# Performance work log

Measured on AMD Instinct MI355X. Metric: run time of the kernel, lower is better.

## Reference

```python
import jax, jax.numpy as jnp
import numpy as np
import math

N_HEADS = 16
DIM = 1024
D_HEAD = DIM // N_HEADS
BS, QLEN = 2, 2048


def setup_inputs() -> dict:
    key = jax.random.key(0)
    ks = jax.random.split(key, 10)
    s = 0.02
    return {
        "input": jax.random.normal(ks[0], (BS, QLEN, DIM), dtype=jnp.float32),
        "mask": jnp.ones((BS, QLEN), dtype=jnp.int32),
        "q_w": jax.random.normal(ks[1], (DIM, DIM), dtype=jnp.float32) * s,
        "q_b": jax.random.normal(ks[2], (DIM,), dtype=jnp.float32) * s,
        "k_w": jax.random.normal(ks[3], (DIM, DIM), dtype=jnp.float32) * s,
        "k_b": jax.random.normal(ks[4], (DIM,), dtype=jnp.float32) * s,
        "v_w": jax.random.normal(ks[5], (DIM, DIM), dtype=jnp.float32) * s,
        "v_b": jax.random.normal(ks[6], (DIM,), dtype=jnp.float32) * s,
        "o_w": jax.random.normal(ks[7], (DIM, DIM), dtype=jnp.float32) * s,
        "o_b": jax.random.normal(ks[8], (DIM,), dtype=jnp.float32) * s,
    }


def _shape(x, bs):
    # (bs, len, dim) -> (bs, heads, len, d_head)
    return x.reshape(bs, -1, N_HEADS, D_HEAD).transpose(0, 2, 1, 3)


def reference(input, mask, q_w, q_b, k_w, k_b, v_w, v_b, o_w, o_b):
    bs, qlen, dim = input.shape
    # projections (torch Linear: x @ W^T + b)
    q = _shape(input @ q_w.T + q_b, bs)
    k = _shape(input @ k_w.T + k_b, bs)
    v = _shape(input @ v_w.T + v_b, bs)
    q = q / math.sqrt(D_HEAD)
    # scores: (bs, heads, qlen, klen)
    scores = jnp.einsum("bhqd,bhkd->bhqk", q, k)
    pad = (mask == 0)[:, None, None, :]  # (bs,1,1,klen)
    scores = jnp.where(pad, -jnp.inf, scores)
    weights = jax.nn.softmax(scores.astype(jnp.float32), axis=-1).astype(scores.dtype)
    # dropout p=0.0 (eval) -> identity
    context = jnp.einsum("bhqk,bhkd->bhqd", weights, v)
    context = context.transpose(0, 2, 1, 3).reshape(bs, qlen, dim)
    return context @ o_w.T + o_b
```

## Files before the change

kernel.cpp:

```cpp
#include <hip/hip_runtime.h>


#define BS    2
#define QLEN  2048
#define DIM   1024
#define NH    16
#define DH    64
#define MTOK  (BS * QLEN)

#define QSCALE 0.18033688011112042f

typedef __attribute__((ext_vector_type(8))) short short8;
typedef __attribute__((ext_vector_type(4))) float float4_t;
typedef __attribute__((ext_vector_type(4))) int   int4_t;

__device__ __forceinline__ ushort f2bf(float f) {
    unsigned u = __float_as_uint(f);
    return (ushort)((u + 0x7fffu + ((u >> 16) & 1u)) >> 16);
}
__device__ __forceinline__ short8 pack8(float4 a0, float4 a1) {
    short8 r;
    r[0] = (short)f2bf(a0.x); r[1] = (short)f2bf(a0.y);
    r[2] = (short)f2bf(a0.z); r[3] = (short)f2bf(a0.w);
    r[4] = (short)f2bf(a1.x); r[5] = (short)f2bf(a1.y);
    r[6] = (short)f2bf(a1.z); r[7] = (short)f2bf(a1.w);
    return r;
}

__device__ __forceinline__ void glds16(const void* g, void* l) {
    __builtin_amdgcn_global_load_lds(
        (const __attribute__((address_space(1))) unsigned int*)g,
        (__attribute__((address_space(3))) unsigned int*)l, 16, 0, 0);
}

#define QBAR() do { asm volatile("" ::: "memory");                            \
                    __builtin_amdgcn_s_barrier();                             \
                    asm volatile("" ::: "memory"); } while (0)

__global__ __launch_bounds__(256) void conv_all(
    const float* __restrict__ x,  const float* __restrict__ qw,
    const float* __restrict__ kw, const float* __restrict__ vw,
    const float* __restrict__ ow,
    ushort* __restrict__ Xbf, ushort* __restrict__ Wbf)
{
    const int blk = blockIdx.x;
    const float* s; ushort* d; size_t base;
    if (blk < 4096)      { s = x;  d = Xbf;             base = (size_t)blk * 1024; }
    else if (blk < 5120) { s = qw; d = Wbf;             base = (size_t)(blk - 4096) * 1024; }
    else if (blk < 6144) { s = kw; d = Wbf + 1048576;   base = (size_t)(blk - 5120) * 1024; }
    else if (blk < 7168) { s = vw; d = Wbf + 2097152;   base = (size_t)(blk - 6144) * 1024; }
    else                 { s = ow; d = Wbf + 3145728;   base = (size_t)(blk - 7168) * 1024; }
    const size_t i = base + threadIdx.x * 4;
    float4 v = *(const float4*)(s + i);
    ushort4 o;
    o.x = f2bf(v.x); o.y = f2bf(v.y); o.z = f2bf(v.z); o.w = f2bf(v.w);
    *(ushort4*)(d + i) = o;
}

__global__ __launch_bounds__(256) void transpose_v(
    const ushort* __restrict__ Vrow, ushort* __restrict__ Vt)
{
    __shared__ ushort T[64][72];
    const int tid  = threadIdx.x;
    const int tile = blockIdx.x;
    const int bh   = blockIdx.y;
    const int b = bh >> 4, h = bh & 15;

    #pragma unroll
    for (int rep = 0; rep < 2; ++rep) {
        int ch = tid + rep * 256;
        int tok = ch >> 3, seg = ch & 7;
        uint4 v = *(const uint4*)(Vrow + (size_t)(b * QLEN + tile * 64 + tok) * DIM
                                        + h * DH + seg * 8);
        *(uint4*)&T[tok][seg * 8] = v;
    }
    __syncthreads();
    #pragma unroll
    for (int rep = 0; rep < 2; ++rep) {
        int ch = tid + rep * 256;
        int dim = ch >> 3, tseg = ch & 7;
        ushort t0 = T[tseg * 8 + 0][dim], t1 = T[tseg * 8 + 1][dim];
        ushort t2 = T[tseg * 8 + 2][dim], t3 = T[tseg * 8 + 3][dim];
        ushort t4 = T[tseg * 8 + 4][dim], t5 = T[tseg * 8 + 5][dim];
        ushort t6 = T[tseg * 8 + 6][dim], t7 = T[tseg * 8 + 7][dim];
        uint4 o;
        o.x = (unsigned)t0 | ((unsigned)t1 << 16);
        o.y = (unsigned)t2 | ((unsigned)t3 << 16);
        o.z = (unsigned)t4 | ((unsigned)t5 << 16);
        o.w = (unsigned)t6 | ((unsigned)t7 << 16);
        *(uint4*)(Vt + (size_t)bh * DH * QLEN + (size_t)dim * QLEN
                      + tile * 64 + tseg * 8) = o;
    }
}

__global__ __launch_bounds__(256) void gemm_qkv(
    const ushort* __restrict__ A, const ushort* __restrict__ Bw,
    const float* __restrict__ bias0, const float* __restrict__ bias1,
    const float* __restrict__ bias2,
    ushort* __restrict__ outQ, ushort* __restrict__ outK, ushort* __restrict__ outVt)
{
    __shared__ ushort As[3][128 * 32];
    __shared__ ushort Bs[3][128 * 32];
    const int tid  = threadIdx.x;
    const int w    = tid >> 6;
    const int lane = tid & 63;
    const int r15  = lane & 15;
    const int quad = lane >> 4;
    const int xcd = blockIdx.x & 7;
    const int lid = blockIdx.x >> 3;
    const int brow = (xcd & 3) * 8  + (lid & 7);
    const int bcol = (xcd >> 2) * 12 + (lid >> 3);
    const int wrow = (w >> 1) * 64;
    const int wcol = (w & 1) * 64;
    const int K = DIM;

    float4_t acc[4][4];
    #pragma unroll
    for (int i = 0; i < 4; ++i)
        #pragma unroll
        for (int j = 0; j < 4; ++j)
            acc[i][j] = (float4_t){0.f, 0.f, 0.f, 0.f};

    int chS[2];
    const ushort* gaS[2];
    const ushort* gbS[2];
    #pragma unroll
    for (int rep = 0; rep < 2; ++rep) {
        const int ch  = w * 128 + rep * 64 + lane;
        const int row = ch >> 2;
        const int g   = (ch & 3) ^ ((row >> 1) & 3);
        chS[rep] = ch;
        gaS[rep] = A  + (size_t)(brow * 128 + row) * K + g * 8;
        gbS[rep] = Bw + (size_t)(bcol * 128 + row) * K + g * 8;
    }
    const int ph = (quad ^ ((r15 >> 1) & 3)) * 8;

#define QKV_STAGE(PS, KOFF) do {                                              \
    _Pragma("unroll")                                                         \
    for (int rep = 0; rep < 2; ++rep) {                                       \
        glds16(gaS[rep] + (KOFF), &As[PS][chS[rep] * 8]);                     \
        glds16(gbS[rep] + (KOFF), &Bs[PS][chS[rep] * 8]);                     \
    }                                                                         \
} while (0)

#define QKV_COMP(PC) do {                                                     \
    short8 af[4], bf[4];                                                      \
    _Pragma("unroll")                                                         \
    for (int ms = 0; ms < 4; ++ms)                                            \
        af[ms] = *(const short8*)&As[PC][(wrow + ms * 16 + r15) * 32 + ph];   \
    _Pragma("unroll")                                                         \
    for (int ns = 0; ns < 4; ++ns)                                            \
        bf[ns] = *(const short8*)&Bs[PC][(wcol + ns * 16 + r15) * 32 + ph];   \
    _Pragma("unroll")                                                         \
    for (int ms = 0; ms < 4; ++ms)                                            \
        _Pragma("unroll")                                                     \
        for (int ns = 0; ns < 4; ++ns)                                        \
            acc[ms][ns] = __builtin_amdgcn_mfma_f32_16x16x32_bf16(            \
                af[ms], bf[ns], acc[ms][ns], 0, 0, 0);                        \
} while (0)

#define QKV_STEP(PC, PS, KOFF2) do {                                          \
    QKV_STAGE(PS, KOFF2);                                                     \
    asm volatile("s_waitcnt vmcnt(8)" ::: "memory");                          \
    __builtin_amdgcn_s_barrier();                                             \
    asm volatile("" ::: "memory");                                            \
    QKV_COMP(PC);                                                             \
    QBAR();                                                                   \
} while (0)

    QKV_STAGE(0, 0);
    QKV_STAGE(1, 32);

    for (int t0 = 0; t0 < 30; t0 += 3) {
        const int kb = t0 * 32;
        QKV_STEP(0, 2, kb + 64);
        QKV_STEP(1, 0, kb + 96);
        QKV_STEP(2, 1, kb + 128);
    }
    asm volatile("s_waitcnt vmcnt(4)" ::: "memory");
    __builtin_amdgcn_s_barrier();
    asm volatile("" ::: "memory");
    QKV_COMP(0);
    QBAR();
    asm volatile("s_waitcnt vmcnt(0)" ::: "memory");
    __builtin_amdgcn_s_barrier();
    asm volatile("" ::: "memory");
    QKV_COMP(1);

#undef QKV_STEP
#undef QKV_COMP
#undef QKV_STAGE

    #pragma unroll
    for (int ms = 0; ms < 4; ++ms) {
        const int rowg = brow * 128 + wrow + ms * 16 + quad * 4;
        #pragma unroll
        for (int ns = 0; ns < 4; ++ns) {
            const int colg = bcol * 128 + wcol + ns * 16 + r15;
            if (colg < 1024) {
                const float bb = bias0[colg];
                #pragma unroll
                for (int r = 0; r < 4; ++r)
                    outQ[(size_t)(rowg + r) * 1024 + colg] =
                        f2bf((acc[ms][ns][r] + bb) * QSCALE);
            } else if (colg < 2048) {
                const float bb = bias1[colg - 1024];
                #pragma unroll
                for (int r = 0; r < 4; ++r)
                    outK[(size_t)(rowg + r) * 1024 + (colg - 1024)] =
                        f2bf(acc[ms][ns][r] + bb);
            } else {
                const int vcol = colg - 2048;
                const int hh = vcol >> 6, dd = vcol & 63;
                const float bb = bias2[vcol];
                const int bidx = rowg >> 11;
                const int tloc = rowg & 2047;
                ushort4 o4;
                o4.x = f2bf(acc[ms][ns][0] + bb);
                o4.y = f2bf(acc[ms][ns][1] + bb);
                o4.z = f2bf(acc[ms][ns][2] + bb);
                o4.w = f2bf(acc[ms][ns][3] + bb);
                *(ushort4*)&outVt[((size_t)(bidx * 16 + hh) * 64 + dd) * QLEN + tloc] = o4;
            }
        }
    }
}

__global__ __launch_bounds__(256) void gemm_o(
    const ushort* __restrict__ A, const ushort* __restrict__ Bw,
    const float* __restrict__ bias, float* __restrict__ Out)
{
    __shared__ ushort As[2][128 * 64];
    __shared__ ushort Bs[2][64 * 64];
    const int tid  = threadIdx.x;
    const int w    = tid >> 6;
    const int lane = tid & 63;
    const int r15  = lane & 15;
    const int quad = lane >> 4;
    const int xcd = blockIdx.x & 7;
    const int lid = blockIdx.x >> 3;
    const int brow = (xcd & 3) * 8 + (lid & 7);
    const int bcol = (xcd >> 2) * 8 + (lid >> 3);
    const int wrow = w * 32;
    const int K = DIM;

    float4_t acc[2][4];
    #pragma unroll
    for (int i = 0; i < 2; ++i)
        #pragma unroll
        for (int j = 0; j < 4; ++j)
            acc[i][j] = (float4_t){0.f, 0.f, 0.f, 0.f};

    int chA[4];  const ushort* gaS[4];
    #pragma unroll
    for (int rep = 0; rep < 4; ++rep) {
        const int ch  = w * 256 + rep * 64 + lane;
        const int row = ch >> 3;
        const int g   = (ch & 7) ^ (row & 7);
        chA[rep] = ch;
        gaS[rep] = A + (size_t)(brow * 128 + row) * K + g * 8;
    }
    int chB[2];  const ushort* gbS[2];
    #pragma unroll
    for (int rep = 0; rep < 2; ++rep) {
        const int ch  = w * 128 + rep * 64 + lane;
        const int row = ch >> 3;
        const int g   = (ch & 7) ^ (row & 7);
        chB[rep] = ch;
        gbS[rep] = Bw + (size_t)(bcol * 64 + row) * K + g * 8;
    }
    const int xg = r15 & 7;

    #pragma unroll
    for (int rep = 0; rep < 4; ++rep)
        glds16(gaS[rep], &As[0][chA[rep] * 8]);
    #pragma unroll
    for (int rep = 0; rep < 2; ++rep)
        glds16(gbS[rep], &Bs[0][chB[rep] * 8]);
    __syncthreads();

    int p = 0;
    for (int k0 = 0; k0 < K; k0 += 64) {
        if (k0 + 64 < K) {
            #pragma unroll
            for (int rep = 0; rep < 4; ++rep)
                glds16(gaS[rep] + k0 + 64, &As[p ^ 1][chA[rep] * 8]);
            #pragma unroll
            for (int rep = 0; rep < 2; ++rep)
                glds16(gbS[rep] + k0 + 64, &Bs[p ^ 1][chB[rep] * 8]);
        }
        #pragma unroll
        for (int hh = 0; hh < 2; ++hh) {
            const int ph = ((hh * 4 + quad) ^ xg) * 8;
            short8 af[2], bf[4];
            #pragma unroll
            for (int ms = 0; ms < 2; ++ms)
                af[ms] = *(const short8*)&As[p][(wrow + ms * 16 + r15) * 64 + ph];
            #pragma unroll
            for (int ns = 0; ns < 4; ++ns)
                bf[ns] = *(const short8*)&Bs[p][(ns * 16 + r15) * 64 + ph];
            #pragma unroll
            for (int ms = 0; ms < 2; ++ms)
                #pragma unroll
                for (int ns = 0; ns < 4; ++ns)
                    acc[ms][ns] = __builtin_amdgcn_mfma_f32_16x16x32_bf16(
                        af[ms], bf[ns], acc[ms][ns], 0, 0, 0);
        }
        __syncthreads();
        p ^= 1;
    }

    #pragma unroll
    for (int ms = 0; ms < 2; ++ms) {
        const int rowg = brow * 128 + wrow + ms * 16 + quad * 4;
        #pragma unroll
        for (int ns = 0; ns < 4; ++ns) {
            const int colg = bcol * 64 + ns * 16 + r15;
            const float bb = bias[colg];
            #pragma unroll
            for (int r = 0; r < 4; ++r)
                Out[(size_t)(rowg + r) * 1024 + colg] = acc[ms][ns][r] + bb;
        }
    }
}

__global__ __launch_bounds__(256) void gemm_f32in_bf16out(
    const float* __restrict__ X, const float* __restrict__ W,
    const float* __restrict__ B, ushort* __restrict__ Out,
    int M, int N, int K, float scale)
{
    const int lane = threadIdx.x & 63;
    const int wid  = (blockIdx.x * blockDim.x + threadIdx.x) >> 6;
    const int tilesN = N >> 4;
    const int tm = wid / tilesN;
    const int tn = wid - tm * tilesN;
    const int r15  = lane & 15;
    const int quad = lane >> 4;

    const float* xp = X + (size_t)(tm * 16 + r15) * K + quad * 8;
    const float* wp = W + (size_t)(tn * 16 + r15) * K + quad * 8;

    float4_t acc = {0.f, 0.f, 0.f, 0.f};
    for (int k0 = 0; k0 < K; k0 += 32) {
        float4 a0 = *(const float4*)(xp + k0);
        float4 a1 = *(const float4*)(xp + k0 + 4);
        float4 b0 = *(const float4*)(wp + k0);
        float4 b1 = *(const float4*)(wp + k0 + 4);
        acc = __builtin_amdgcn_mfma_f32_16x16x32_bf16(pack8(a0, a1), pack8(b0, b1), acc, 0, 0, 0);
    }
    const int col  = tn * 16 + r15;
    const float bias = B[col];
    const int row0 = tm * 16 + quad * 4;
    #pragma unroll
    for (int r = 0; r < 4; ++r)
        Out[(size_t)(row0 + r) * N + col] = f2bf((acc[r] + bias) * scale);
}

__global__ __launch_bounds__(256) void gemm_bf16in_f32out(
    const ushort* __restrict__ X, const float* __restrict__ W,
    const float* __restrict__ B, float* __restrict__ Out,
    int M, int N, int K)
{
    const int lane = threadIdx.x & 63;
    const int wid  = (blockIdx.x * blockDim.x + threadIdx.x) >> 6;
    const int tilesN = N >> 4;
    const int tm = wid / tilesN;
    const int tn = wid - tm * tilesN;
    const int r15  = lane & 15;
    const int quad = lane >> 4;

    const ushort* xp = X + (size_t)(tm * 16 + r15) * K + quad * 8;
    const float*  wp = W + (size_t)(tn * 16 + r15) * K + quad * 8;

    float4_t acc = {0.f, 0.f, 0.f, 0.f};
    for (int k0 = 0; k0 < K; k0 += 32) {
        short8 a = *(const short8*)(xp + k0);
        float4 b0 = *(const float4*)(wp + k0);
        float4 b1 = *(const float4*)(wp + k0 + 4);
        acc = __builtin_amdgcn_mfma_f32_16x16x32_bf16(a, pack8(b0, b1), acc, 0, 0, 0);
    }
    const int col  = tn * 16 + r15;
    const float bias = B[col];
    const int row0 = tm * 16 + quad * 4;
    #pragma unroll
    for (int r = 0; r < 4; ++r)
        Out[(size_t)(row0 + r) * N + col] = acc[r] + bias;
}

__global__ __launch_bounds__(256, 2) void flash_attn(
    const ushort* __restrict__ Qb, const ushort* __restrict__ Kb,
    const ushort* __restrict__ Vt, const int* __restrict__ mask,
    ushort* __restrict__ Cb)
{
    __shared__ __align__(16) ushort Ks[2][64][64];
    __shared__ __align__(16) ushort Vs[4][64][64];
    __shared__ __align__(16) float  Mb[QLEN];

    const int tid  = threadIdx.x;
    const int w    = tid >> 6;
    const int lane = tid & 63;
    const int r15  = lane & 15;
    const int quad = lane >> 4;
    const int flat = blockIdx.x;
    const int xcd  = flat & 7;
    const int j    = flat >> 3;
    const int bh   = xcd + 8 * (j >> 4);
    const int qt   = j & 15;
    const int b = bh >> 4, h = bh & 15;

    {
        const int4* m4 = (const int4*)(mask + b * QLEN);
        #pragma unroll
        for (int rep = 0; rep < 2; ++rep) {
            const int idx = tid + rep * 256;
            int4 mv = m4[idx];
            float4 o;
            o.x = mv.x ? 0.f : -INFINITY;
            o.y = mv.y ? 0.f : -INFINITY;
            o.z = mv.z ? 0.f : -INFINITY;
            o.w = mv.w ? 0.f : -INFINITY;
            *(float4*)&Mb[idx * 4] = o;
        }
    }

    const int qbase = qt * 128 + w * 32;
    const ushort* qp = Qb + (size_t)(b * QLEN + qbase + r15) * DIM + h * DH + quad * 8;
    short8 qf[2][2];
    qf[0][0] = *(const short8*)(qp);
    qf[0][1] = *(const short8*)(qp + 32);
    qf[1][0] = *(const short8*)(qp + 16 * DIM);
    qf[1][1] = *(const short8*)(qp + 16 * DIM + 32);

    const ushort* kg = Kb + (size_t)b * QLEN * DIM + h * DH;
    const ushort* vg = Vt + (size_t)bh * DH * QLEN;

    const int a0 = tid >> 3, seg = tid & 7;
    const int krow0 = (((a0 & 7) >> 2) << 4) + (((a0 >> 3) & 3) << 2) + (a0 & 3);
    const int sK = (seg ^ (krow0 & 7)) << 3;
    const int sV = (seg ^ (a0 & 7)) << 3;
    const int xq = (quad ^ (r15 & 7)) << 3;

    float4_t o[2][4];
    float4_t ol[2];
    #pragma unroll
    for (int rg = 0; rg < 2; ++rg) {
        ol[rg] = (float4_t){0.f, 0.f, 0.f, 0.f};
        #pragma unroll
        for (int ds = 0; ds < 4; ++ds)
            o[rg][ds] = (float4_t){0.f, 0.f, 0.f, 0.f};
    }
    short8 ones8;
    #pragma unroll
    for (int i = 0; i < 8; ++i) ones8[i] = (short)0x3F80;

    uint4 kr0, kr1, vr0, vr1;
    int pkA[4][2][2], pkB[4][2][2];

#define LOAD_TILE(KT) do {                                                    \
    kr0 = *(const uint4*)(kg + (size_t)((KT) + a0     ) * DIM  + seg * 8);    \
    kr1 = *(const uint4*)(kg + (size_t)((KT) + a0 + 32) * DIM  + seg * 8);    \
    vr0 = *(const uint4*)(vg + (size_t)(a0     ) * QLEN + (KT) + seg * 8);    \
    vr1 = *(const uint4*)(vg + (size_t)(a0 + 32) * QLEN + (KT) + seg * 8);    \
} while (0)

#define STORE_TILE(KBUF, VBUF) do {                                           \
    *(uint4*)&Ks[KBUF][krow0     ][sK] = kr0;                                 \
    *(uint4*)&Ks[KBUF][krow0 + 32][sK] = kr1;                                 \
    *(uint4*)&Vs[VBUF][a0        ][sV] = vr0;                                 \
    *(uint4*)&Vs[VBUF][a0 + 32   ][sV] = vr1;                                 \
} while (0)

#define S_PHASE(KBUF, KT, PK) do {                                            \
    _Pragma("unroll")                                                         \
    for (int ks = 0; ks < 4; ++ks) {                                          \
        const ushort* krow = &Ks[KBUF][ks * 16 + r15][0];                     \
        short8 kf0 = *(const short8*)(krow + xq);                             \
        short8 kf1 = *(const short8*)(krow + (xq ^ 32));                      \
        const float4 mb = *(const float4*)&Mb[(KT) + ((ks >> 1) << 5)         \
                                              + (quad << 3) + ((ks & 1) << 2)]; \
        _Pragma("unroll")                                                     \
        for (int rg = 0; rg < 2; ++rg) {                                      \
            float4_t s = {0.f, 0.f, 0.f, 0.f};                                \
            s = __builtin_amdgcn_mfma_f32_16x16x32_bf16(kf0, qf[rg][0], s, 0, 0, 0); \
            s = __builtin_amdgcn_mfma_f32_16x16x32_bf16(kf1, qf[rg][1], s, 0, 0, 0); \
            unsigned u0 = __float_as_uint(__builtin_amdgcn_exp2f(s[0] + mb.x)); \
            unsigned u1 = __float_as_uint(__builtin_amdgcn_exp2f(s[1] + mb.y)); \
            unsigned u2 = __float_as_uint(__builtin_amdgcn_exp2f(s[2] + mb.z)); \
            unsigned u3 = __float_as_uint(__builtin_amdgcn_exp2f(s[3] + mb.w)); \
            PK[ks][rg][0] = __builtin_amdgcn_perm(u1, u0, 0x07060302);        \
            PK[ks][rg][1] = __builtin_amdgcn_perm(u3, u2, 0x07060302);        \
        }                                                                     \
    }                                                                         \
} while (0)

#define PV_PHASE(VBUF, PK) do {                                               \
    _Pragma("unroll")                                                         \
    for (int ck = 0; ck < 2; ++ck) {                                          \
        short8 vf[4];                                                         \
        _Pragma("unroll")                                                     \
        for (int ds = 0; ds < 4; ++ds)                                        \
            vf[ds] = *(const short8*)(&Vs[VBUF][ds * 16 + r15][0] + (xq ^ (ck << 5))); \
        _Pragma("unroll")                                                     \
        for (int rg = 0; rg < 2; ++rg) {                                      \
            int4_t pfi = { PK[2 * ck][rg][0], PK[2 * ck][rg][1],              \
                           PK[2 * ck + 1][rg][0], PK[2 * ck + 1][rg][1] };    \
            short8 pf = __builtin_bit_cast(short8, pfi);                      \
            _Pragma("unroll")                                                 \
            for (int ds = 0; ds < 4; ++ds)                                    \
                o[rg][ds] = __builtin_amdgcn_mfma_f32_16x16x32_bf16(          \
                    pf, vf[ds], o[rg][ds], 0, 0, 0);                          \
            ol[rg] = __builtin_amdgcn_mfma_f32_16x16x32_bf16(                 \
                pf, ones8, ol[rg], 0, 0, 0);                                  \
        }                                                                     \
    }                                                                         \
} while (0)

    LOAD_TILE(0);
    STORE_TILE(0, 0);
    LOAD_TILE(64);
    __syncthreads();
    S_PHASE(0, 0, pkA);
    STORE_TILE(1, 1);
    __syncthreads();
    LOAD_TILE(128);

    for (int kb = 0; kb < 1792; kb += 256) {
        S_PHASE(1, kb + 64, pkB);  PV_PHASE(0, pkA);
        STORE_TILE(0, 2); __syncthreads(); LOAD_TILE(kb + 192);
        S_PHASE(0, kb + 128, pkA); PV_PHASE(1, pkB);
        STORE_TILE(1, 3); __syncthreads(); LOAD_TILE(kb + 256);
        S_PHASE(1, kb + 192, pkB); PV_PHASE(2, pkA);
        STORE_TILE(0, 0); __syncthreads(); LOAD_TILE(kb + 320);
        S_PHASE(0, kb + 256, pkA); PV_PHASE(3, pkB);
        STORE_TILE(1, 1); __syncthreads(); LOAD_TILE(kb + 384);
    }

    S_PHASE(1, 1856, pkB); PV_PHASE(0, pkA);
    STORE_TILE(0, 2); __syncthreads(); LOAD_TILE(1984);
    S_PHASE(0, 1920, pkA); PV_PHASE(1, pkB);
    STORE_TILE(1, 3); __syncthreads();
    S_PHASE(1, 1984, pkB); PV_PHASE(2, pkA);
    PV_PHASE(3, pkB);

#undef LOAD_TILE
#undef STORE_TILE
#undef S_PHASE
#undef PV_PHASE

    #pragma unroll
    for (int rg = 0; rg < 2; ++rg) {
        #pragma unroll
        for (int r = 0; r < 4; ++r) {
            const float ir = 1.f / fmaxf(ol[rg][r], 1e-30f);
            const size_t rb = (size_t)(b * QLEN + qbase + rg * 16 + quad * 4 + r) * DIM
                              + h * DH;
            Cb[rb +  0 + r15] = f2bf(o[rg][0][r] * ir);
            Cb[rb + 16 + r15] = f2bf(o[rg][1][r] * ir);
            Cb[rb + 32 + r15] = f2bf(o[rg][2][r] * ir);
            Cb[rb + 48 + r15] = f2bf(o[rg][3][r] * ir);
        }
    }
}

extern "C" void kernel_launch(void* const* d_in, const int* in_sizes, int n_in,
                              void* d_out, int out_size, void* d_ws, size_t ws_size,
                              hipStream_t stream)
{
    const float* x    = (const float*)d_in[0];
    const int*   mask = (const int*)d_in[1];
    const float* q_w  = (const float*)d_in[2];
    const float* q_b  = (const float*)d_in[3];
    const float* k_w  = (const float*)d_in[4];
    const float* k_b  = (const float*)d_in[5];
    const float* v_w  = (const float*)d_in[6];
    const float* v_b  = (const float*)d_in[7];
    const float* o_w  = (const float*)d_in[8];
    const float* o_b  = (const float*)d_in[9];
    float* out = (float*)d_out;

    const size_t SEG = (size_t)MTOK * DIM;
    ushort* Qbf = (ushort*)d_out;
    ushort* Xbf = Qbf + SEG;
    ushort* Kb  = (ushort*)d_ws;
    ushort* Cb  = Kb + SEG;
    ushort* Vt  = Cb + SEG;
    ushort* Wbf = Vt + SEG;

    const bool big = ws_size >= (size_t)32 * 1024 * 1024;

    if (big) {
        conv_all<<<8192, 256, 0, stream>>>(x, q_w, k_w, v_w, o_w, Xbf, Wbf);
        gemm_qkv<<<(MTOK / 128) * (3072 / 128), 256, 0, stream>>>(
            Xbf, Wbf, q_b, k_b, v_b, Qbf, Kb, Vt);
        flash_attn<<<(QLEN / 128) * (BS * NH), 256, 0, stream>>>(Qbf, Kb, Vt, mask, Cb);
        gemm_o<<<(MTOK / 128) * (DIM / 64), 256, 0, stream>>>(
            Cb, Wbf + 3 * (size_t)(DIM * DIM), o_b, out);
    } else {
        const int tiles   = (MTOK / 16) * (DIM / 16);
        const int gblocks = tiles / 4;
        gemm_f32in_bf16out<<<gblocks, 256, 0, stream>>>(x, q_w, q_b, Qbf, MTOK, DIM, DIM, QSCALE);
        gemm_f32in_bf16out<<<gblocks, 256, 0, stream>>>(x, k_w, k_b, Kb,  MTOK, DIM, DIM, 1.0f);
        gemm_f32in_bf16out<<<gblocks, 256, 0, stream>>>(x, v_w, v_b, Cb,  MTOK, DIM, DIM, 1.0f);
        transpose_v<<<dim3(QLEN / 64, BS * NH), 256, 0, stream>>>(Cb, Vt);
        flash_attn<<<(QLEN / 128) * (BS * NH), 256, 0, stream>>>(Qbf, Kb, Vt, mask, Cb);
        gemm_bf16in_f32out<<<tiles / 4, 256, 0, stream>>>(Cb, o_w, o_b, out, MTOK, DIM, DIM);
    }
}
```

Measured before the change: 196.3 us.

## Enlarge QKV GEMM tiles to 256x256 with 512 threads and phased MFMA schedule

```diff
diff --git a/kernel.cpp b/kernel.cpp
--- a/kernel.cpp
+++ b/kernel.cpp
@@ -32,10 +32,6 @@
         (const __attribute__((address_space(1))) unsigned int*)g,
         (__attribute__((address_space(3))) unsigned int*)l, 16, 0, 0);
 }
-
-#define QBAR() do { asm volatile("" ::: "memory");                            \
-                    __builtin_amdgcn_s_barrier();                             \
-                    asm volatile("" ::: "memory"); } while (0)
 
 __global__ __launch_bounds__(256) void conv_all(
     const float* __restrict__ x,  const float* __restrict__ qw,
@@ -93,134 +89,156 @@
     }
 }
 
-__global__ __launch_bounds__(256) void gemm_qkv(
+__global__ __launch_bounds__(512, 2) void gemm_qkv(
     const ushort* __restrict__ A, const ushort* __restrict__ Bw,
     const float* __restrict__ bias0, const float* __restrict__ bias1,
     const float* __restrict__ bias2,
     ushort* __restrict__ outQ, ushort* __restrict__ outK, ushort* __restrict__ outVt)
 {
-    __shared__ ushort As[3][128 * 32];
-    __shared__ ushort Bs[3][128 * 32];
+    __shared__ ushort As[2][256 * 64];
+    __shared__ ushort Bs[2][256 * 64];
+
     const int tid  = threadIdx.x;
     const int w    = tid >> 6;
     const int lane = tid & 63;
     const int r15  = lane & 15;
     const int quad = lane >> 4;
+    const int wm   = w >> 2;
+    const int wn   = w & 3;
+    const int xg   = r15 & 7;
+
     const int xcd = blockIdx.x & 7;
     const int lid = blockIdx.x >> 3;
-    const int brow = (xcd & 3) * 8  + (lid & 7);
-    const int bcol = (xcd >> 2) * 12 + (lid >> 3);
-    const int wrow = (w >> 1) * 64;
-    const int wcol = (w & 1) * 64;
+    const int brow = (xcd & 3) * 4 + (lid & 3);
+    const int bcol = (xcd >> 2) * 6 + (lid >> 2);
     const int K = DIM;
 
-    float4_t acc[4][4];
-    #pragma unroll
-    for (int i = 0; i < 4; ++i)
+    float4_t acc[8][4];
+    #pragma unroll
+    for (int i = 0; i < 8; ++i)
         #pragma unroll
         for (int j = 0; j < 4; ++j)
             acc[i][j] = (float4_t){0.f, 0.f, 0.f, 0.f};
 
-    int chS[2];
-    const ushort* gaS[2];
-    const ushort* gbS[2];
-    #pragma unroll
-    for (int rep = 0; rep < 2; ++rep) {
-        const int ch  = w * 128 + rep * 64 + lane;
-        const int row = ch >> 2;
-        const int g   = (ch & 3) ^ ((row >> 1) & 3);
-        chS[rep] = ch;
-        gaS[rep] = A  + (size_t)(brow * 128 + row) * K + g * 8;
-        gbS[rep] = Bw + (size_t)(bcol * 128 + row) * K + g * 8;
-    }
-    const int ph = (quad ^ ((r15 >> 1) & 3)) * 8;
-
-#define QKV_STAGE(PS, KOFF) do {                                              \
+    const ushort* gaS[4];
+    const ushort* gbS[4];
+    #pragma unroll
+    for (int rep = 0; rep < 4; ++rep) {
+        const int c   = rep * 512 + tid;
+        const int row = c >> 3;
+        const int g   = (c & 7) ^ (row & 7);
+        gaS[rep] = A  + (size_t)(brow * 256 + row) * K + g * 8;
+        gbS[rep] = Bw + (size_t)(bcol * 256 + row) * K + g * 8;
+    }
+
+#define QBAR() do { asm volatile("" ::: "memory");                            \
+                    __builtin_amdgcn_s_barrier();                             \
+                    asm volatile("" ::: "memory"); } while (0)
+#define QVM0() asm volatile("s_waitcnt vmcnt(0)" ::: "memory")
+
+#define STAGE_T(BUFI, KOFF) do {                                              \
     _Pragma("unroll")                                                         \
-    for (int rep = 0; rep < 2; ++rep) {                                       \
-        glds16(gaS[rep] + (KOFF), &As[PS][chS[rep] * 8]);                     \
-        glds16(gbS[rep] + (KOFF), &Bs[PS][chS[rep] * 8]);                     \
+    for (int rep = 0; rep < 4; ++rep) {                                       \
+        glds16(gaS[rep] + (KOFF), &As[BUFI][(rep * 512 + tid) * 8]);          \
+        glds16(gbS[rep] + (KOFF), &Bs[BUFI][(rep * 512 + tid) * 8]);          \
     }                                                                         \
 } while (0)
 
-#define QKV_COMP(PC) do {                                                     \
-    short8 af[4], bf[4];                                                      \
+    short8 afr[2][4];
+
+#define PH_A(BUFI, MH) do {                                                   \
+    const int arow0 = wm * 128 + (MH) * 64;                                   \
     _Pragma("unroll")                                                         \
-    for (int ms = 0; ms < 4; ++ms)                                            \
-        af[ms] = *(const short8*)&As[PC][(wrow + ms * 16 + r15) * 32 + ph];   \
+    for (int hh = 0; hh < 2; ++hh) {                                          \
+        const int ph = ((hh * 4 + quad) ^ xg) * 8;                            \
+        _Pragma("unroll")                                                     \
+        for (int ms = 0; ms < 4; ++ms)                                        \
+            afr[hh][ms] = *(const short8*)&As[BUFI][(arow0 + ms * 16 + r15) * 64 + ph]; \
+    }                                                                         \
+} while (0)
+
+#define PH_BM(BUFI, MH, NH) do {                                              \
+    const int bcol0 = wn * 64 + (NH) * 32;                                    \
+    short8 bfr[2][2];                                                         \
     _Pragma("unroll")                                                         \
-    for (int ns = 0; ns < 4; ++ns)                                            \
-        bf[ns] = *(const short8*)&Bs[PC][(wcol + ns * 16 + r15) * 32 + ph];   \
+    for (int hh = 0; hh < 2; ++hh) {                                          \
+        const int ph = ((hh * 4 + quad) ^ xg) * 8;                            \
+        _Pragma("unroll")                                                     \
+        for (int ns = 0; ns < 2; ++ns)                                        \
+            bfr[hh][ns] = *(const short8*)&Bs[BUFI][(bcol0 + ns * 16 + r15) * 64 + ph]; \
+    }                                                                         \
+    __builtin_amdgcn_s_setprio(1);                                            \
     _Pragma("unroll")                                                         \
-    for (int ms = 0; ms < 4; ++ms)                                            \
+    for (int hh = 0; hh < 2; ++hh)                                            \
         _Pragma("unroll")                                                     \
-        for (int ns = 0; ns < 4; ++ns)                                        \
-            acc[ms][ns] = __builtin_amdgcn_mfma_f32_16x16x32_bf16(            \
-                af[ms], bf[ns], acc[ms][ns], 0, 0, 0);                        \
-} while (0)
-
-#define QKV_STEP(PC, PS, KOFF2) do {                                          \
-    QKV_STAGE(PS, KOFF2);                                                     \
-    asm volatile("s_waitcnt vmcnt(8)" ::: "memory");                          \
-    __builtin_amdgcn_s_barrier();                                             \
-    asm volatile("" ::: "memory");                                            \
-    QKV_COMP(PC);                                                             \
-    QBAR();                                                                   \
-} while (0)
-
-    QKV_STAGE(0, 0);
-    QKV_STAGE(1, 32);
-
-    for (int t0 = 0; t0 < 30; t0 += 3) {
-        const int kb = t0 * 32;
-        QKV_STEP(0, 2, kb + 64);
-        QKV_STEP(1, 0, kb + 96);
-        QKV_STEP(2, 1, kb + 128);
-    }
-    asm volatile("s_waitcnt vmcnt(4)" ::: "memory");
-    __builtin_amdgcn_s_barrier();
-    asm volatile("" ::: "memory");
-    QKV_COMP(0);
+        for (int ms = 0; ms < 4; ++ms)                                        \
+            _Pragma("unroll")                                                  \
+            for (int ns = 0; ns < 2; ++ns)                                    \
+                acc[(MH) * 4 + ms][(NH) * 2 + ns] =                           \
+                    __builtin_amdgcn_mfma_f32_16x16x32_bf16(                  \
+                        afr[hh][ms], bfr[hh][ns],                             \
+                        acc[(MH) * 4 + ms][(NH) * 2 + ns], 0, 0, 0);          \
+    __builtin_amdgcn_s_setprio(0);                                            \
+} while (0)
+
+#define QITER(KB, LAST) do {                                                  \
+    STAGE_T(1, (KB) + 64);                                                    \
+    PH_A(0, 0); PH_BM(0, 0, 0);            QBAR();                            \
+    PH_BM(0, 0, 1);                        QBAR();                            \
+    PH_A(0, 1); PH_BM(0, 1, 0);            QBAR();                            \
+    PH_BM(0, 1, 1); QVM0();                QBAR();                            \
+    if (!(LAST)) STAGE_T(0, (KB) + 128);                                      \
+    PH_A(1, 0); PH_BM(1, 0, 0);            QBAR();                            \
+    PH_BM(1, 0, 1);                        QBAR();                            \
+    PH_A(1, 1); PH_BM(1, 1, 0);            QBAR();                            \
+    PH_BM(1, 1, 1); if (!(LAST)) { QVM0(); } QBAR();                          \
+} while (0)
+
+    STAGE_T(0, 0);
+    QVM0();
     QBAR();
-    asm volatile("s_waitcnt vmcnt(0)" ::: "memory");
-    __builtin_amdgcn_s_barrier();
-    asm volatile("" ::: "memory");
-    QKV_COMP(1);
-
-#undef QKV_STEP
-#undef QKV_COMP
-#undef QKV_STAGE
-
-    #pragma unroll
-    for (int ms = 0; ms < 4; ++ms) {
-        const int rowg = brow * 128 + wrow + ms * 16 + quad * 4;
-        #pragma unroll
-        for (int ns = 0; ns < 4; ++ns) {
-            const int colg = bcol * 128 + wcol + ns * 16 + r15;
+
+    for (int i = 0; i < 7; ++i)
+        QITER(i * 128, 0);
+    QITER(896, 1);
+
+#undef QITER
+#undef PH_BM
+#undef PH_A
+#undef STAGE_T
+#undef QVM0
+#undef QBAR
+
+    #pragma unroll
+    for (int msg = 0; msg < 8; ++msg) {
+        const int rowg = brow * 256 + wm * 128 + msg * 16 + quad * 4;
+        #pragma unroll
+        for (int nsg = 0; nsg < 4; ++nsg) {
+            const int colg = bcol * 256 + wn * 64 + nsg * 16 + r15;
             if (colg < 1024) {
                 const float bb = bias0[colg];
                 #pragma unroll
                 for (int r = 0; r < 4; ++r)
                     outQ[(size_t)(rowg + r) * 1024 + colg] =
-                        f2bf((acc[ms][ns][r] + bb) * QSCALE);
+                        f2bf((acc[msg][nsg][r] + bb) * QSCALE);
             } else if (colg < 2048) {
                 const float bb = bias1[colg - 1024];
                 #pragma unroll
                 for (int r = 0; r < 4; ++r)
                     outK[(size_t)(rowg + r) * 1024 + (colg - 1024)] =
-                        f2bf(acc[ms][ns][r] + bb);
+                        f2bf(acc[msg][nsg][r] + bb);
             } else {
                 const int vcol = colg - 2048;
-                const int hh = vcol >> 6, dd = vcol & 63;
+                const int hh2 = vcol >> 6, dd = vcol & 63;
                 const float bb = bias2[vcol];
                 const int bidx = rowg >> 11;
                 const int tloc = rowg & 2047;
                 ushort4 o4;
-                o4.x = f2bf(acc[ms][ns][0] + bb);
-                o4.y = f2bf(acc[ms][ns][1] + bb);
-                o4.z = f2bf(acc[ms][ns][2] + bb);
-                o4.w = f2bf(acc[ms][ns][3] + bb);
-                *(ushort4*)&outVt[((size_t)(bidx * 16 + hh) * 64 + dd) * QLEN + tloc] = o4;
+                o4.x = f2bf(acc[msg][nsg][0] + bb);
+                o4.y = f2bf(acc[msg][nsg][1] + bb);
+                o4.z = f2bf(acc[msg][nsg][2] + bb);
+                o4.w = f2bf(acc[msg][nsg][3] + bb);
+                *(ushort4*)&outVt[((size_t)(bidx * 16 + hh2) * 64 + dd) * QLEN + tloc] = o4;
             }
         }
     }
@@ -590,7 +608,7 @@
 
     if (big) {
         conv_all<<<8192, 256, 0, stream>>>(x, q_w, k_w, v_w, o_w, Xbf, Wbf);
-        gemm_qkv<<<(MTOK / 128) * (3072 / 128), 256, 0, stream>>>(
+        gemm_qkv<<<(MTOK / 256) * (3072 / 256), 512, 0, stream>>>(
             Xbf, Wbf, q_b, k_b, v_b, Qbf, Kb, Vt);
         flash_attn<<<(QLEN / 128) * (BS * NH), 256, 0, stream>>>(Qbf, Kb, Vt, mask, Cb);
         gemm_o<<<(MTOK / 128) * (DIM / 64), 256, 0, stream>>>(
```

After: 195.2 us. No clear change (-0.6%).
